# Optimization experiments

Hardware: AMD Instinct MI355X
Metric: run time of the kernel (lower is better)

The kernel has to match this reference:

```python
import jax, jax.numpy as jnp
import numpy as np

# MoE config (matches init_kwargs)
DMODEL = 1024
N_EXPERTS = 32
EXPERT_SIZE = 512
N_HEADS = 4  # top-k experts per token
WEIGHT_SCALE = 1.0


def setup_inputs() -> dict:
    key = jax.random.key(0)
    k0, k1, k2, k3 = jax.random.split(key, 4)
    x = jax.random.normal(k0, (2, 2048, DMODEL), dtype=jnp.float32)
    # expert selection keys: [n_experts, dmodel], std = dmodel**-0.5
    expert_sel = jax.random.normal(k1, (N_EXPERTS, DMODEL), dtype=jnp.float32) * (DMODEL ** -0.5)
    # expert input keys: [n_experts, dmodel, expert_size], std = dmodel**-0.5
    keys = jax.random.normal(k2, (N_EXPERTS, DMODEL, EXPERT_SIZE), dtype=jnp.float32) * (DMODEL ** -0.5)
    # expert output values: [n_experts, expert_size, v_dim], std = (n_experts*expert_size)**-0.5
    values = jax.random.normal(k3, (N_EXPERTS, EXPERT_SIZE, DMODEL), dtype=jnp.float32) * ((N_EXPERTS * EXPERT_SIZE) ** -0.5)
    return {"x": x, "expert_sel": expert_sel, "keys": keys, "values": values}


def reference(x, expert_sel, keys, values):
    # x: [B, S, D]
    B, S, D = x.shape
    xt = x.reshape(-1, D)                      # [N, D] tokens
    N = xt.shape[0]

    # --- routing: sigmoid gating + top-k expert selection ---
    sel_logits = jnp.einsum('nd,ed->ne', xt, expert_sel)   # [N, E]
    gates = jax.nn.sigmoid(sel_logits)                     # [N, E]
    sel_val, sel_idx = jax.lax.top_k(gates, N_HEADS)       # [N, K]

    # scatter selected gate values into a dense [N, E] gate matrix
    # (zero gate for non-selected experts == gather/scatter of expert MLPs)
    gate_full = jnp.zeros_like(gates).at[jnp.arange(N)[:, None], sel_idx].set(sel_val)

    # --- expert MLP: key scores -> ReLU -> gate-weighted -> value combine ---
    scores = jax.nn.relu(jnp.einsum('nd,edf->nef', xt, keys))   # [N, E, F]
    scores = scores * gate_full[:, :, None]                     # mask + sigmoid gate
    out = jnp.einsum('nef,efv->nv', scores, values)             # [N, V]

    return out.reshape(B, S, -1)
```

## Files before the change

kernel.cpp:

```cpp
#include <hip/hip_runtime.h>

#define DMODEL 1024
#define NEXP   32
#define FDIM   512
#define TOPK   4

#define MT    128
#define NT    128
#define BK    32
#define RTB   8
#define NBORD 64

using short8 = __attribute__((ext_vector_type(8))) short;
using f32x4  = __attribute__((ext_vector_type(4))) float;

#define AS1 __attribute__((address_space(1)))
#define AS3 __attribute__((address_space(3)))
__device__ __forceinline__ void gload_lds16(const void* g, void* l) {
    __builtin_amdgcn_global_load_lds((const AS1 unsigned int*)g, (AS3 unsigned int*)l, 16, 0, 0);
}

__device__ __forceinline__ unsigned short f2b(float f) {
    unsigned int u = __float_as_uint(f);
    unsigned int r = (u + 0x7FFFu + ((u >> 16) & 1u)) >> 16;
    return (unsigned short)r;
}

__global__ __launch_bounds__(256) void route_a(
    const float* __restrict__ x, const float* __restrict__ esel,
    unsigned short* __restrict__ xb,
    unsigned int* __restrict__ sel_e, float* __restrict__ sel_g, int ntok)
{
    int tile0 = blockIdx.x * RTB;
    int tid = threadIdx.x;

    __shared__ float xs[RTB][DMODEL];
    __shared__ float gs[RTB][NEXP];

    {
        const float4* src = (const float4*)(x + (size_t)tile0 * DMODEL);
        float4* dst = (float4*)&xs[0][0];
        int navail = min(RTB, ntok - tile0) * (DMODEL / 4);
        for (int i = tid; i < RTB * (DMODEL / 4); i += 256)
            dst[i] = src[i < navail ? i : 0];
    }
    __syncthreads();

    int e = tid >> 3, sub = tid & 7;
    float4 acc0 = {0,0,0,0}, acc1 = {0,0,0,0}, acc2 = {0,0,0,0}, acc3 = {0,0,0,0};
    float4 acc4 = {0,0,0,0}, acc5 = {0,0,0,0}, acc6 = {0,0,0,0}, acc7 = {0,0,0,0};
    const float* er = esel + (size_t)e * DMODEL + sub * 4;
    #pragma unroll 4
    for (int j = 0; j < DMODEL / 32; j++) {
        float4 ev = *(const float4*)(er + j * 32);
        int kk = sub * 4 + j * 32;
        float4 x0 = *(const float4*)(&xs[0][kk]);
        float4 x1 = *(const float4*)(&xs[1][kk]);
        float4 x2 = *(const float4*)(&xs[2][kk]);
        float4 x3 = *(const float4*)(&xs[3][kk]);
        float4 x4 = *(const float4*)(&xs[4][kk]);
        float4 x5 = *(const float4*)(&xs[5][kk]);
        float4 x6 = *(const float4*)(&xs[6][kk]);
        float4 x7 = *(const float4*)(&xs[7][kk]);
        acc0.x += ev.x*x0.x; acc0.y += ev.y*x0.y; acc0.z += ev.z*x0.z; acc0.w += ev.w*x0.w;
        acc1.x += ev.x*x1.x; acc1.y += ev.y*x1.y; acc1.z += ev.z*x1.z; acc1.w += ev.w*x1.w;
        acc2.x += ev.x*x2.x; acc2.y += ev.y*x2.y; acc2.z += ev.z*x2.z; acc2.w += ev.w*x2.w;
        acc3.x += ev.x*x3.x; acc3.y += ev.y*x3.y; acc3.z += ev.z*x3.z; acc3.w += ev.w*x3.w;
        acc4.x += ev.x*x4.x; acc4.y += ev.y*x4.y; acc4.z += ev.z*x4.z; acc4.w += ev.w*x4.w;
        acc5.x += ev.x*x5.x; acc5.y += ev.y*x5.y; acc5.z += ev.z*x5.z; acc5.w += ev.w*x5.w;
        acc6.x += ev.x*x6.x; acc6.y += ev.y*x6.y; acc6.z += ev.z*x6.z; acc6.w += ev.w*x6.w;
        acc7.x += ev.x*x7.x; acc7.y += ev.y*x7.y; acc7.z += ev.z*x7.z; acc7.w += ev.w*x7.w;
    }
    {
        float s[RTB] = {
            acc0.x+acc0.y+acc0.z+acc0.w, acc1.x+acc1.y+acc1.z+acc1.w,
            acc2.x+acc2.y+acc2.z+acc2.w, acc3.x+acc3.y+acc3.z+acc3.w,
            acc4.x+acc4.y+acc4.z+acc4.w, acc5.x+acc5.y+acc5.z+acc5.w,
            acc6.x+acc6.y+acc6.z+acc6.w, acc7.x+acc7.y+acc7.z+acc7.w };
        #pragma unroll
        for (int t = 0; t < RTB; t++) {
            float v = s[t];
            v += __shfl_xor(v, 1);
            v += __shfl_xor(v, 2);
            v += __shfl_xor(v, 4);
            if (sub == 0) gs[t][e] = 1.f / (1.f + expf(-v));
        }
    }
    __syncthreads();

    {
        int t = tid >> 5, e2 = tid & 31;
        int tok = tile0 + t;
        if (tok < ntok) {
            float v = gs[t][e2];
            #pragma unroll
            for (int r = 0; r < TOPK; r++) {
                float bv = v; int bi = e2;
                #pragma unroll
                for (int sft = 16; sft >= 1; sft >>= 1) {
                    float ov = __shfl_xor(bv, sft, 32);
                    int   oi = __shfl_xor(bi, sft, 32);
                    if (ov > bv || (ov == bv && oi < bi)) { bv = ov; bi = oi; }
                }
                if (e2 == bi) v = -1e30f;
                if (e2 == r) {
                    sel_e[(size_t)tok * TOPK + r] = (unsigned)bi;
                    sel_g[(size_t)tok * TOPK + r] = bv;
                }
            }
        }
    }

    {
        int navail = min(RTB, ntok - tile0) * (DMODEL / 4);
        ushort4* dst = (ushort4*)(xb + (size_t)tile0 * DMODEL);
        const float4* srcl = (const float4*)&xs[0][0];
        for (int i = tid; i < navail; i += 256) {
            float4 v = srcl[i];
            ushort4 o;
            o.x = f2b(v.x); o.y = f2b(v.y); o.z = f2b(v.z); o.w = f2b(v.w);
            dst[i] = o;
        }
    }
}

__global__ __launch_bounds__(256) void hist_k(
    const unsigned int* __restrict__ sel_e, int* __restrict__ ghist, int nsel)
{
    __shared__ int h[NEXP];
    int tid = threadIdx.x;
    if (tid < NEXP) h[tid] = 0;
    __syncthreads();
    int chunk = (nsel + gridDim.x - 1) / gridDim.x;
    int i0 = blockIdx.x * chunk, i1 = min(i0 + chunk, nsel);
    for (int i = i0 + tid; i < i1; i += 256)
        atomicAdd(&h[sel_e[i]], 1);
    __syncthreads();
    if (tid < NEXP) ghist[blockIdx.x * NEXP + tid] = h[tid];
}

__global__ __launch_bounds__(64) void scan2_k(
    const int* __restrict__ ghist, int* __restrict__ goff,
    int* __restrict__ counts, int* __restrict__ base,
    int* __restrict__ tiles, int* __restrict__ ntiles, int nb)
{
    int e = threadIdx.x;
    if (e < NEXP) {
        int s = 0;
        for (int b = 0; b < nb; b++) {
            goff[b * NEXP + e] = s;
            s += ghist[b * NEXP + e];
        }
        counts[e] = s;
    }
    __syncthreads();
    if (e == 0) {
        int s = 0, nt = 0;
        for (int e2 = 0; e2 < NEXP; e2++) {
            base[e2] = s;
            int c = counts[e2];
            for (int t0 = 0; t0 < c; t0 += MT) tiles[nt++] = (e2 << 8) | (t0 / MT);
            s += c;
        }
        *ntiles = nt;
    }
}

__global__ __launch_bounds__(256) void scat_k(
    const unsigned int* __restrict__ sel_e, const float* __restrict__ sel_g,
    const int* __restrict__ goff,
    int* __restrict__ tok_list, float* __restrict__ gate_list,
    unsigned int* __restrict__ slotinfo, int nsel, int ntok)
{
    __shared__ int c[NEXP];
    int tid = threadIdx.x;
    if (tid < NEXP) c[tid] = goff[blockIdx.x * NEXP + tid];
    __syncthreads();
    int chunk = (nsel + gridDim.x - 1) / gridDim.x;
    int i0 = blockIdx.x * chunk, i1 = min(i0 + chunk, nsel);
    for (int i = i0 + tid; i < i1; i += 256) {
        unsigned int e = sel_e[i];
        float g = sel_g[i];
        int pos = atomicAdd(&c[e], 1);
        tok_list [(size_t)e * ntok + pos] = i >> 2;
        gate_list[(size_t)e * ntok + pos] = g;
        slotinfo[i] = (e << 16) | (unsigned)pos;
    }
}

__global__ __launch_bounds__(256) void prep_t(const float* __restrict__ src,
                                              unsigned short* __restrict__ dst,
                                              int R, int C) {
    __shared__ float tile[64][65];
    int e  = blockIdx.z;
    int r0 = blockIdx.y * 64, c0 = blockIdx.x * 64;
    const float* s = src + (size_t)e * R * C;
    unsigned short* d = dst + (size_t)e * R * C;
    for (int i = 0; i < 16; i++) {
        int c = i * 256 + threadIdx.x;
        int rr = c >> 6, cc = c & 63;
        tile[rr][cc] = s[(size_t)(r0 + rr) * C + c0 + cc];
    }
    __syncthreads();
    for (int i = 0; i < 16; i++) {
        int c = i * 256 + threadIdx.x;
        int wr = c >> 6, wc = c & 63;
        d[(size_t)(c0 + wr) * R + r0 + wc] = f2b(tile[wc][wr]);
    }
}

__global__ __launch_bounds__(256) void gemm1_k(
    const unsigned short* __restrict__ xb,
    const unsigned short* __restrict__ kt,
    const int* __restrict__ counts, const int* __restrict__ base,
    const int* __restrict__ tiles, const int* __restrict__ ntiles,
    const int* __restrict__ tok_list, const float* __restrict__ gate_list,
    unsigned short* __restrict__ hs, int ntok)
{
    int ti = blockIdx.x;
    if (ti >= *ntiles) return;
    int code = tiles[ti];
    int e = code >> 8, t0 = (code & 255) * MT;
    int cnt  = counts[e];
    int f0   = blockIdx.y * NT;
    int live = min(MT, cnt - t0);

    __shared__ unsigned short Xs[MT * BK];
    __shared__ unsigned short Ks[NT * BK];
    __shared__ int   toks[MT];
    __shared__ float gts[MT];

    int tid = threadIdx.x, lane = tid & 63, w = tid >> 6;
    int lr = lane & 15, lg = lane >> 4;

    if (tid < MT) {
        bool lv = tid < live;
        toks[tid] = lv ? tok_list [(size_t)e * ntok + t0 + tid] : 0;
        gts[tid]  = lv ? gate_list[(size_t)e * ntok + t0 + tid] : 0.f;
    }
    __syncthreads();

    int c0c = 2 * w, c1c = 2 * w + 1;
    int rowA = c0c * 16 + (lane >> 2);
    int rowB = c1c * 16 + (lane >> 2);
    int qq   = (lane & 3) * 8;
    const unsigned short* ke = kt + (size_t)e * FDIM * DMODEL + (size_t)f0 * DMODEL;
    const unsigned short* sx0 = xb + (size_t)toks[rowA] * DMODEL + qq;
    const unsigned short* sx1 = xb + (size_t)toks[rowB] * DMODEL + qq;
    const unsigned short* sk0 = ke + (size_t)rowA * DMODEL + qq;
    const unsigned short* sk1 = ke + (size_t)rowB * DMODEL + qq;
    unsigned short* dx0 = Xs + c0c * 512;
    unsigned short* dx1 = Xs + c1c * 512;
    unsigned short* dk0 = Ks + c0c * 512;
    unsigned short* dk1 = Ks + c1c * 512;

    f32x4 acc[8][2];
    #pragma unroll
    for (int m = 0; m < 8; m++)
        #pragma unroll
        for (int n = 0; n < 2; n++)
            acc[m][n] = (f32x4){0.f, 0.f, 0.f, 0.f};

    for (int k0 = 0; k0 < DMODEL; k0 += BK) {
        gload_lds16(sx0 + k0, dx0);
        gload_lds16(sx1 + k0, dx1);
        gload_lds16(sk0 + k0, dk0);
        gload_lds16(sk1 + k0, dk1);
        __syncthreads();
        short8 a[8];
        #pragma unroll
        for (int m = 0; m < 8; m++)
            a[m] = *(const short8*)(Xs + (m * 16 + lr) * BK + lg * 8);
        #pragma unroll
        for (int n = 0; n < 2; n++) {
            short8 b = *(const short8*)(Ks + (w * 32 + n * 16 + lr) * BK + lg * 8);
            #pragma unroll
            for (int m = 0; m < 8; m++)
                acc[m][n] = __builtin_amdgcn_mfma_f32_16x16x32_bf16(a[m], b, acc[m][n], 0, 0, 0);
        }
        __syncthreads();
    }

    int hb = base[e] + t0;
    #pragma unroll
    for (int m = 0; m < 8; m++) {
        #pragma unroll
        for (int n = 0; n < 2; n++) {
            int col = f0 + w * 32 + n * 16 + lr;
            #pragma unroll
            for (int r = 0; r < 4; r++) {
                int row = m * 16 + lg * 4 + r;
                if (row < live)
                    hs[(size_t)(hb + row) * FDIM + col] = f2b(fmaxf(acc[m][n][r], 0.f) * gts[row]);
            }
        }
    }
}

__global__ __launch_bounds__(256) void gemm2_k(
    const unsigned short* __restrict__ hs,
    const unsigned short* __restrict__ vt,
    const int* __restrict__ counts, const int* __restrict__ base,
    const int* __restrict__ tiles, const int* __restrict__ ntiles,
    float* __restrict__ ys)
{
    int ti = blockIdx.x;
    if (ti >= *ntiles) return;
    int code = tiles[ti];
    int e = code >> 8, t0 = (code & 255) * MT;
    int cnt  = counts[e];
    int v0   = blockIdx.y * NT;
    int live = min(MT, cnt - t0);
    int hb   = base[e] + t0;

    __shared__ unsigned short Hs[MT * BK];
    __shared__ unsigned short Vs[NT * BK];

    int tid = threadIdx.x, lane = tid & 63, w = tid >> 6;
    int lr = lane & 15, lg = lane >> 4;

    int c0c = 2 * w, c1c = 2 * w + 1;
    int rowA = c0c * 16 + (lane >> 2);
    int rowB = c1c * 16 + (lane >> 2);
    int qq   = (lane & 3) * 8;
    const unsigned short* he = hs + (size_t)hb * FDIM;
    const unsigned short* ve = vt + (size_t)e * DMODEL * FDIM + (size_t)v0 * FDIM;
    const unsigned short* sh0 = he + (size_t)rowA * FDIM + qq;
    const unsigned short* sh1 = he + (size_t)rowB * FDIM + qq;
    const unsigned short* sv0 = ve + (size_t)rowA * FDIM + qq;
    const unsigned short* sv1 = ve + (size_t)rowB * FDIM + qq;
    unsigned short* dh0 = Hs + c0c * 512;
    unsigned short* dh1 = Hs + c1c * 512;
    unsigned short* dv0 = Vs + c0c * 512;
    unsigned short* dv1 = Vs + c1c * 512;

    f32x4 acc[8][2];
    #pragma unroll
    for (int m = 0; m < 8; m++)
        #pragma unroll
        for (int n = 0; n < 2; n++)
            acc[m][n] = (f32x4){0.f, 0.f, 0.f, 0.f};

    for (int k0 = 0; k0 < FDIM; k0 += BK) {
        gload_lds16(sh0 + k0, dh0);
        gload_lds16(sh1 + k0, dh1);
        gload_lds16(sv0 + k0, dv0);
        gload_lds16(sv1 + k0, dv1);
        __syncthreads();
        short8 a[8];
        #pragma unroll
        for (int m = 0; m < 8; m++)
            a[m] = *(const short8*)(Hs + (m * 16 + lr) * BK + lg * 8);
        #pragma unroll
        for (int n = 0; n < 2; n++) {
            short8 b = *(const short8*)(Vs + (w * 32 + n * 16 + lr) * BK + lg * 8);
            #pragma unroll
            for (int m = 0; m < 8; m++)
                acc[m][n] = __builtin_amdgcn_mfma_f32_16x16x32_bf16(a[m], b, acc[m][n], 0, 0, 0);
        }
        __syncthreads();
    }

    #pragma unroll
    for (int m = 0; m < 8; m++) {
        #pragma unroll
        for (int n = 0; n < 2; n++) {
            int col = v0 + w * 32 + n * 16 + lr;
            #pragma unroll
            for (int r = 0; r < 4; r++) {
                int row = m * 16 + lg * 4 + r;
                if (row < live)
                    ys[(size_t)(hb + row) * DMODEL + col] = acc[m][n][r];
            }
        }
    }
}

__global__ __launch_bounds__(256) void combine_k(
    const float* __restrict__ ys, const unsigned int* __restrict__ slotinfo,
    const int* __restrict__ base, float* __restrict__ out)
{
    int tok = blockIdx.x;
    unsigned int s0 = slotinfo[(size_t)tok * TOPK + 0];
    unsigned int s1 = slotinfo[(size_t)tok * TOPK + 1];
    unsigned int s2 = slotinfo[(size_t)tok * TOPK + 2];
    unsigned int s3 = slotinfo[(size_t)tok * TOPK + 3];
    const float4* y0 = (const float4*)(ys + (size_t)(base[s0 >> 16] + (s0 & 0xFFFF)) * DMODEL);
    const float4* y1 = (const float4*)(ys + (size_t)(base[s1 >> 16] + (s1 & 0xFFFF)) * DMODEL);
    const float4* y2 = (const float4*)(ys + (size_t)(base[s2 >> 16] + (s2 & 0xFFFF)) * DMODEL);
    const float4* y3 = (const float4*)(ys + (size_t)(base[s3 >> 16] + (s3 & 0xFFFF)) * DMODEL);
    int i = threadIdx.x;
    float4 a = y0[i], b = y1[i], c = y2[i], d = y3[i];
    float4 o;
    o.x = a.x + b.x + c.x + d.x;
    o.y = a.y + b.y + c.y + d.y;
    o.z = a.z + b.z + c.z + d.z;
    o.w = a.w + b.w + c.w + d.w;
    ((float4*)(out + (size_t)tok * DMODEL))[i] = o;
}

#define BTF 16
__global__ __launch_bounds__(256) void expert_k(
    const float* __restrict__ x, const float* __restrict__ keys,
    const float* __restrict__ values, const int* __restrict__ counts,
    const int* __restrict__ tok_list, const float* __restrict__ gate_list,
    float* __restrict__ out, int ntok)
{
    int e   = blockIdx.y;
    int cnt = counts[e];
    int t0  = blockIdx.x * BTF;
    if (t0 >= cnt) return;
    int nt = (cnt - t0 < BTF) ? (cnt - t0) : BTF;

    __shared__ float xs[BTF][DMODEL];
    __shared__ float hsl[BTF][FDIM];
    __shared__ int   toks[BTF];
    __shared__ float gts[BTF];

    if (threadIdx.x < BTF) {
        int t = threadIdx.x;
        bool live = (t < nt);
        toks[t] = live ? tok_list [(size_t)e * ntok + t0 + t] : 0;
        gts[t]  = live ? gate_list[(size_t)e * ntok + t0 + t] : 0.f;
    }
    __syncthreads();
    for (int i = threadIdx.x; i < BTF * (DMODEL / 4); i += 256) {
        int r = i >> 8, c = i & 255;
        ((float4*)xs[r])[c] = ((const float4*)(x + (size_t)toks[r] * DMODEL))[c];
    }
    __syncthreads();

    {
        int f = threadIdx.x * 2;
        float acc0[BTF], acc1[BTF];
        #pragma unroll
        for (int t = 0; t < BTF; t++) { acc0[t] = 0.f; acc1[t] = 0.f; }
        const float* kp = keys + (size_t)e * DMODEL * FDIM + f;
        for (int k = 0; k < DMODEL; k += 4) {
            const float* kr = kp + (size_t)k * FDIM;
            float2 kv0 = *(const float2*)(kr);
            float2 kv1 = *(const float2*)(kr + FDIM);
            float2 kv2 = *(const float2*)(kr + 2 * FDIM);
            float2 kv3 = *(const float2*)(kr + 3 * FDIM);
            #pragma unroll
            for (int t = 0; t < BTF; t++) {
                float4 xv = *(const float4*)(&xs[t][k]);
                acc0[t] += xv.x * kv0.x + xv.y * kv1.x + xv.z * kv2.x + xv.w * kv3.x;
                acc1[t] += xv.x * kv0.y + xv.y * kv1.y + xv.z * kv2.y + xv.w * kv3.y;
            }
        }
        #pragma unroll
        for (int t = 0; t < BTF; t++) {
            float g = gts[t];
            hsl[t][f]     = fmaxf(acc0[t], 0.f) * g;
            hsl[t][f + 1] = fmaxf(acc1[t], 0.f) * g;
        }
    }
    __syncthreads();

    {
        int v = threadIdx.x * 4;
        float acc[BTF][4];
        #pragma unroll
        for (int t = 0; t < BTF; t++) { acc[t][0]=0.f; acc[t][1]=0.f; acc[t][2]=0.f; acc[t][3]=0.f; }
        const float* vp = values + (size_t)e * FDIM * DMODEL + v;
        for (int k = 0; k < FDIM; k += 2) {
            float4 va0 = *(const float4*)(vp + (size_t)k * DMODEL);
            float4 va1 = *(const float4*)(vp + (size_t)(k + 1) * DMODEL);
            #pragma unroll
            for (int t = 0; t < BTF; t++) {
                float2 hv = *(const float2*)(&hsl[t][k]);
                acc[t][0] += hv.x * va0.x + hv.y * va1.x;
                acc[t][1] += hv.x * va0.y + hv.y * va1.y;
                acc[t][2] += hv.x * va0.z + hv.y * va1.z;
                acc[t][3] += hv.x * va0.w + hv.y * va1.w;
            }
        }
        #pragma unroll
        for (int t = 0; t < BTF; t++) {
            if (t < nt) {
                float* orow = out + (size_t)toks[t] * DMODEL + v;
                atomicAdd(orow + 0, acc[t][0]);
                atomicAdd(orow + 1, acc[t][1]);
                atomicAdd(orow + 2, acc[t][2]);
                atomicAdd(orow + 3, acc[t][3]);
            }
        }
    }
}

extern "C" void kernel_launch(void* const* d_in, const int* in_sizes, int n_in,
                              void* d_out, int out_size, void* d_ws, size_t ws_size,
                              hipStream_t stream) {
    const float* x      = (const float*)d_in[0];
    const float* esel   = (const float*)d_in[1];
    const float* keys   = (const float*)d_in[2];
    const float* values = (const float*)d_in[3];
    float* out = (float*)d_out;
    int ntok = in_sizes[0] / DMODEL;

    const size_t OFF_BASE = 512;
    const size_t OFF_NT   = 1024;
    const size_t OFF_TILE = 2048;
    const size_t OFF_HIST = 16 << 10;
    const size_t OFF_GOFF = 32 << 10;
    const size_t OFF_SLOT = 64 << 10;
    const size_t OFF_SELE = 128 << 10;
    const size_t OFF_SELG = 192 << 10;
    const size_t OFF_TOK  = 256 << 10;
    const size_t OFF_GATE = 1ull << 20;
    const size_t OFF_XB   = 2ull << 20;
    const size_t OFF_KT   = 12ull << 20;
    const size_t OFF_VT   = 46ull << 20;
    const size_t OFF_HS   = 80ull << 20;
    const size_t OFF_YS   = 98ull << 20;
    const size_t NEED     = OFF_YS + (size_t)ntok * TOPK * DMODEL * sizeof(float) + (1 << 20);

    int*      counts    = (int*)d_ws;
    int*      ebase     = (int*)((char*)d_ws + OFF_BASE);
    int*      ntiles    = (int*)((char*)d_ws + OFF_NT);
    int*      tiles     = (int*)((char*)d_ws + OFF_TILE);
    int*      ghist     = (int*)((char*)d_ws + OFF_HIST);
    int*      goff      = (int*)((char*)d_ws + OFF_GOFF);
    unsigned* slotinfo  = (unsigned*)((char*)d_ws + OFF_SLOT);
    unsigned* sel_e     = (unsigned*)((char*)d_ws + OFF_SELE);
    float*    sel_g     = (float*)((char*)d_ws + OFF_SELG);
    int*      tok_list  = (int*)((char*)d_ws + OFF_TOK);
    float*    gate_list = (float*)((char*)d_ws + OFF_GATE);
    unsigned short* xb  = (unsigned short*)((char*)d_ws + OFF_XB);

    int nsel = ntok * TOPK;
    int rblocks = (ntok + RTB - 1) / RTB;
    route_a<<<rblocks, 256, 0, stream>>>(x, esel, xb, sel_e, sel_g, ntok);
    hist_k<<<NBORD, 256, 0, stream>>>(sel_e, ghist, nsel);
    scan2_k<<<1, 64, 0, stream>>>(ghist, goff, counts, ebase, tiles, ntiles, NBORD);
    scat_k<<<NBORD, 256, 0, stream>>>(sel_e, sel_g, goff, tok_list, gate_list,
                                      slotinfo, nsel, ntok);

    if (ws_size >= NEED) {
        unsigned short* kt = (unsigned short*)((char*)d_ws + OFF_KT);
        unsigned short* vt = (unsigned short*)((char*)d_ws + OFF_VT);
        unsigned short* hs = (unsigned short*)((char*)d_ws + OFF_HS);
        float*          ys = (float*)((char*)d_ws + OFF_YS);

        prep_t<<<dim3(FDIM / 64, DMODEL / 64, NEXP), 256, 0, stream>>>(keys,   kt, DMODEL, FDIM);
        prep_t<<<dim3(DMODEL / 64, FDIM / 64, NEXP), 256, 0, stream>>>(values, vt, FDIM, DMODEL);

        int maxt = (ntok * TOPK + MT - 1) / MT + NEXP;
        gemm1_k<<<dim3(maxt, FDIM / NT), 256, 0, stream>>>(
            xb, kt, counts, ebase, tiles, ntiles, tok_list, gate_list, hs, ntok);
        gemm2_k<<<dim3(maxt, DMODEL / NT), 256, 0, stream>>>(
            hs, vt, counts, ebase, tiles, ntiles, ys);
        combine_k<<<ntok, 256, 0, stream>>>(ys, slotinfo, ebase, out);
    } else {
        hipMemsetAsync(out, 0, (size_t)out_size * sizeof(float), stream);
        int ntiles2 = (ntok + BTF - 1) / BTF;
        expert_k<<<dim3(ntiles2, NEXP), 256, 0, stream>>>(
            x, keys, values, counts, tok_list, gate_list, out, ntok);
    }
}
```

Before: 202.2 us.

## Double K-tile to 64 with XOR-swizzled LDS and store expert outputs as bf16

Both expert GEMMs now load a 64-wide K slice per iteration. Each LDS chunk holds 8 rows by 64 columns, and the column chunk index is XOR-swizzled by row to avoid bank conflicts on the fragment reads. This halves the number of barrier pairs per K loop. Separately, the per-slot expert outputs ys are written as bf16 instead of fp32, halving the bytes written by gemm2 and read by combine, at the cost of extra rounding before the top-k sum.

Result: faster. 196.5 us (-2.8%).

```diff
diff --git a/kernel.cpp b/kernel.cpp
--- a/kernel.cpp
+++ b/kernel.cpp
@@ -7,7 +7,7 @@
 
 #define MT    128
 #define NT    128
-#define BK    32
+#define BK    64
 #define RTB   8
 #define NBORD 64
 
@@ -24,6 +24,9 @@
     unsigned int u = __float_as_uint(f);
     unsigned int r = (u + 0x7FFFu + ((u >> 16) & 1u)) >> 16;
     return (unsigned short)r;
+}
+__device__ __forceinline__ float b2f(unsigned short u) {
+    return __uint_as_float((unsigned int)u << 16);
 }
 
 __global__ __launch_bounds__(256) void route_a(
@@ -240,19 +243,22 @@
     }
     __syncthreads();
 
-    int c0c = 2 * w, c1c = 2 * w + 1;
-    int rowA = c0c * 16 + (lane >> 2);
-    int rowB = c1c * 16 + (lane >> 2);
-    int qq   = (lane & 3) * 8;
+    int lrow = lane >> 3;
+    int scol = ((lane & 7) ^ lrow) * 8;
     const unsigned short* ke = kt + (size_t)e * FDIM * DMODEL + (size_t)f0 * DMODEL;
-    const unsigned short* sx0 = xb + (size_t)toks[rowA] * DMODEL + qq;
-    const unsigned short* sx1 = xb + (size_t)toks[rowB] * DMODEL + qq;
-    const unsigned short* sk0 = ke + (size_t)rowA * DMODEL + qq;
-    const unsigned short* sk1 = ke + (size_t)rowB * DMODEL + qq;
-    unsigned short* dx0 = Xs + c0c * 512;
-    unsigned short* dx1 = Xs + c1c * 512;
-    unsigned short* dk0 = Ks + c0c * 512;
-    unsigned short* dk1 = Ks + c1c * 512;
+    const unsigned short* sx[4];
+    const unsigned short* sk[4];
+    unsigned short* dx[4];
+    unsigned short* dk[4];
+    #pragma unroll
+    for (int j = 0; j < 4; j++) {
+        int ch = 4 * w + j;
+        int row = ch * 8 + lrow;
+        sx[j] = xb + (size_t)toks[row] * DMODEL + scol;
+        sk[j] = ke + (size_t)row * DMODEL + scol;
+        dx[j] = Xs + ch * 512;
+        dk[j] = Ks + ch * 512;
+    }
 
     f32x4 acc[8][2];
     #pragma unroll
@@ -262,21 +268,28 @@
             acc[m][n] = (f32x4){0.f, 0.f, 0.f, 0.f};
 
     for (int k0 = 0; k0 < DMODEL; k0 += BK) {
-        gload_lds16(sx0 + k0, dx0);
-        gload_lds16(sx1 + k0, dx1);
-        gload_lds16(sk0 + k0, dk0);
-        gload_lds16(sk1 + k0, dk1);
+        #pragma unroll
+        for (int j = 0; j < 4; j++) {
+            gload_lds16(sx[j] + k0, dx[j]);
+            gload_lds16(sk[j] + k0, dk[j]);
+        }
         __syncthreads();
-        short8 a[8];
-        #pragma unroll
-        for (int m = 0; m < 8; m++)
-            a[m] = *(const short8*)(Xs + (m * 16 + lr) * BK + lg * 8);
-        #pragma unroll
-        for (int n = 0; n < 2; n++) {
-            short8 b = *(const short8*)(Ks + (w * 32 + n * 16 + lr) * BK + lg * 8);
-            #pragma unroll
-            for (int m = 0; m < 8; m++)
-                acc[m][n] = __builtin_amdgcn_mfma_f32_16x16x32_bf16(a[m], b, acc[m][n], 0, 0, 0);
+        #pragma unroll
+        for (int ks = 0; ks < 2; ks++) {
+            short8 a[8];
+            #pragma unroll
+            for (int m = 0; m < 8; m++) {
+                int row = m * 16 + lr;
+                a[m] = *(const short8*)(Xs + row * BK + (((ks * 4 + lg) ^ (lr & 7)) * 8));
+            }
+            #pragma unroll
+            for (int n = 0; n < 2; n++) {
+                int row = w * 32 + n * 16 + lr;
+                short8 b = *(const short8*)(Ks + row * BK + (((ks * 4 + lg) ^ (lr & 7)) * 8));
+                #pragma unroll
+                for (int m = 0; m < 8; m++)
+                    acc[m][n] = __builtin_amdgcn_mfma_f32_16x16x32_bf16(a[m], b, acc[m][n], 0, 0, 0);
+            }
         }
         __syncthreads();
     }
@@ -302,7 +315,7 @@
     const unsigned short* __restrict__ vt,
     const int* __restrict__ counts, const int* __restrict__ base,
     const int* __restrict__ tiles, const int* __restrict__ ntiles,
-    float* __restrict__ ys)
+    unsigned short* __restrict__ ys)
 {
     int ti = blockIdx.x;
     if (ti >= *ntiles) return;
@@ -319,20 +332,23 @@
     int tid = threadIdx.x, lane = tid & 63, w = tid >> 6;
     int lr = lane & 15, lg = lane >> 4;
 
-    int c0c = 2 * w, c1c = 2 * w + 1;
-    int rowA = c0c * 16 + (lane >> 2);
-    int rowB = c1c * 16 + (lane >> 2);
-    int qq   = (lane & 3) * 8;
+    int lrow = lane >> 3;
+    int scol = ((lane & 7) ^ lrow) * 8;
     const unsigned short* he = hs + (size_t)hb * FDIM;
     const unsigned short* ve = vt + (size_t)e * DMODEL * FDIM + (size_t)v0 * FDIM;
-    const unsigned short* sh0 = he + (size_t)rowA * FDIM + qq;
-    const unsigned short* sh1 = he + (size_t)rowB * FDIM + qq;
-    const unsigned short* sv0 = ve + (size_t)rowA * FDIM + qq;
-    const unsigned short* sv1 = ve + (size_t)rowB * FDIM + qq;
-    unsigned short* dh0 = Hs + c0c * 512;
-    unsigned short* dh1 = Hs + c1c * 512;
-    unsigned short* dv0 = Vs + c0c * 512;
-    unsigned short* dv1 = Vs + c1c * 512;
+    const unsigned short* sh[4];
+    const unsigned short* sv[4];
+    unsigned short* dh[4];
+    unsigned short* dv[4];
+    #pragma unroll
+    for (int j = 0; j < 4; j++) {
+        int ch = 4 * w + j;
+        int row = ch * 8 + lrow;
+        sh[j] = he + (size_t)row * FDIM + scol;
+        sv[j] = ve + (size_t)row * FDIM + scol;
+        dh[j] = Hs + ch * 512;
+        dv[j] = Vs + ch * 512;
+    }
 
     f32x4 acc[8][2];
     #pragma unroll
@@ -342,21 +358,28 @@
             acc[m][n] = (f32x4){0.f, 0.f, 0.f, 0.f};
 
     for (int k0 = 0; k0 < FDIM; k0 += BK) {
-        gload_lds16(sh0 + k0, dh0);
-        gload_lds16(sh1 + k0, dh1);
-        gload_lds16(sv0 + k0, dv0);
-        gload_lds16(sv1 + k0, dv1);
+        #pragma unroll
+        for (int j = 0; j < 4; j++) {
+            gload_lds16(sh[j] + k0, dh[j]);
+            gload_lds16(sv[j] + k0, dv[j]);
+        }
         __syncthreads();
-        short8 a[8];
-        #pragma unroll
-        for (int m = 0; m < 8; m++)
-            a[m] = *(const short8*)(Hs + (m * 16 + lr) * BK + lg * 8);
-        #pragma unroll
-        for (int n = 0; n < 2; n++) {
-            short8 b = *(const short8*)(Vs + (w * 32 + n * 16 + lr) * BK + lg * 8);
-            #pragma unroll
-            for (int m = 0; m < 8; m++)
-                acc[m][n] = __builtin_amdgcn_mfma_f32_16x16x32_bf16(a[m], b, acc[m][n], 0, 0, 0);
+        #pragma unroll
+        for (int ks = 0; ks < 2; ks++) {
+            short8 a[8];
+            #pragma unroll
+            for (int m = 0; m < 8; m++) {
+                int row = m * 16 + lr;
+                a[m] = *(const short8*)(Hs + row * BK + (((ks * 4 + lg) ^ (lr & 7)) * 8));
+            }
+            #pragma unroll
+            for (int n = 0; n < 2; n++) {
+                int row = w * 32 + n * 16 + lr;
+                short8 b = *(const short8*)(Vs + row * BK + (((ks * 4 + lg) ^ (lr & 7)) * 8));
+                #pragma unroll
+                for (int m = 0; m < 8; m++)
+                    acc[m][n] = __builtin_amdgcn_mfma_f32_16x16x32_bf16(a[m], b, acc[m][n], 0, 0, 0);
+            }
         }
         __syncthreads();
     }
@@ -370,14 +393,14 @@
             for (int r = 0; r < 4; r++) {
                 int row = m * 16 + lg * 4 + r;
                 if (row < live)
-                    ys[(size_t)(hb + row) * DMODEL + col] = acc[m][n][r];
+                    ys[(size_t)(hb + row) * DMODEL + col] = f2b(acc[m][n][r]);
             }
         }
     }
 }
 
 __global__ __launch_bounds__(256) void combine_k(
-    const float* __restrict__ ys, const unsigned int* __restrict__ slotinfo,
+    const unsigned short* __restrict__ ys, const unsigned int* __restrict__ slotinfo,
     const int* __restrict__ base, float* __restrict__ out)
 {
     int tok = blockIdx.x;
@@ -385,17 +408,17 @@
     unsigned int s1 = slotinfo[(size_t)tok * TOPK + 1];
     unsigned int s2 = slotinfo[(size_t)tok * TOPK + 2];
     unsigned int s3 = slotinfo[(size_t)tok * TOPK + 3];
-    const float4* y0 = (const float4*)(ys + (size_t)(base[s0 >> 16] + (s0 & 0xFFFF)) * DMODEL);
-    const float4* y1 = (const float4*)(ys + (size_t)(base[s1 >> 16] + (s1 & 0xFFFF)) * DMODEL);
-    const float4* y2 = (const float4*)(ys + (size_t)(base[s2 >> 16] + (s2 & 0xFFFF)) * DMODEL);
-    const float4* y3 = (const float4*)(ys + (size_t)(base[s3 >> 16] + (s3 & 0xFFFF)) * DMODEL);
+    const ushort4* y0 = (const ushort4*)(ys + (size_t)(base[s0 >> 16] + (s0 & 0xFFFF)) * DMODEL);
+    const ushort4* y1 = (const ushort4*)(ys + (size_t)(base[s1 >> 16] + (s1 & 0xFFFF)) * DMODEL);
+    const ushort4* y2 = (const ushort4*)(ys + (size_t)(base[s2 >> 16] + (s2 & 0xFFFF)) * DMODEL);
+    const ushort4* y3 = (const ushort4*)(ys + (size_t)(base[s3 >> 16] + (s3 & 0xFFFF)) * DMODEL);
     int i = threadIdx.x;
-    float4 a = y0[i], b = y1[i], c = y2[i], d = y3[i];
+    ushort4 a = y0[i], b = y1[i], c = y2[i], d = y3[i];
     float4 o;
-    o.x = a.x + b.x + c.x + d.x;
-    o.y = a.y + b.y + c.y + d.y;
-    o.z = a.z + b.z + c.z + d.z;
-    o.w = a.w + b.w + c.w + d.w;
+    o.x = b2f(a.x) + b2f(b.x) + b2f(c.x) + b2f(d.x);
+    o.y = b2f(a.y) + b2f(b.y) + b2f(c.y) + b2f(d.y);
+    o.z = b2f(a.z) + b2f(b.z) + b2f(c.z) + b2f(d.z);
+    o.w = b2f(a.w) + b2f(b.w) + b2f(c.w) + b2f(d.w);
     ((float4*)(out + (size_t)tok * DMODEL))[i] = o;
 }
 
@@ -541,7 +564,7 @@
         unsigned short* kt = (unsigned short*)((char*)d_ws + OFF_KT);
         unsigned short* vt = (unsigned short*)((char*)d_ws + OFF_VT);
         unsigned short* hs = (unsigned short*)((char*)d_ws + OFF_HS);
-        float*          ys = (float*)((char*)d_ws + OFF_YS);
+        unsigned short* ys = (unsigned short*)((char*)d_ws + OFF_YS);
 
         prep_t<<<dim3(FDIM / 64, DMODEL / 64, NEXP), 256, 0, stream>>>(keys,   kt, DMODEL, FDIM);
         prep_t<<<dim3(DMODEL / 64, FDIM / 64, NEXP), 256, 0, stream>>>(values, vt, FDIM, DMODEL);
```
